# Performance work log

Hardware: AMD Instinct MI355X
Metric: run time of the kernel (lower is better)

Reference implementation:

```python
import jax, jax.numpy as jnp
import numpy as np

# NF4 quantization levels (16 entries) from NF4Quantizer
NF4_LEVELS = jnp.array([
    -1.0, -0.6961928009986877, -0.5250730514526367, -0.39491748809814453,
    -0.28444138169288635, -0.18477343022823334, -0.09105003625154495, 0.0,
    0.07958029955625534, 0.16093020141124725, 0.24611230194568634,
    0.33791524171829224, 0.44070982933044434, 0.5626170039176941,
    0.7229568362236023, 1.0], dtype=jnp.float32)

OUT_F, IN_F = 4096, 4096
B, S = 2, 512

def setup_inputs() -> dict:
    key = jax.random.key(0)
    k1, k2, k3, k4, k5 = jax.random.split(key, 5)
    x = jax.random.normal(k1, (B, S, IN_F), dtype=jnp.float32)
    w0 = jax.random.normal(k2, (OUT_F, IN_F), dtype=jnp.float32) * 0.02
    nf4_idx = jax.random.randint(k3, (OUT_F, IN_F), 0, 16, dtype=jnp.int32)
    scale = jax.random.uniform(k4, (1,), dtype=jnp.float32) * 0.1 + 0.01
    zero_point = jax.random.normal(k5, (1,), dtype=jnp.float32) * 0.01
    return {"x": x, "w0": w0, "nf4_idx": nf4_idx, "scale": scale,
            "zero_point": zero_point}

def reference(x, w0, nf4_idx, scale, zero_point):
    # NF4 dequantize: look up level values, then affine (quantized*scale + zp)
    q = NF4_LEVELS[nf4_idx]                      # [out, in] float32
    deq_w = q * scale + zero_point               # dequantized adaptor weight
    # frozen base linear + dequantized low-rank-adaptor linear (QLoRA-style)
    base = jnp.einsum('bsi,oi->bso', x, w0)
    adapt = jnp.einsum('bsi,oi->bso', x, deq_w)
    return base + adapt
```

## Files before the change

### kernel.cpp

```cpp
#include <hip/hip_runtime.h>
#include <hip/hip_bf16.h>
#include <stdint.h>

#define MDIM 1024
#define NDIM 4096
#define KDIM 4096

#define BM 128
#define BN 128
#define BK 64

typedef __attribute__((ext_vector_type(4))) float f32x4;
typedef __attribute__((ext_vector_type(4))) float float4v;
typedef __attribute__((ext_vector_type(4))) int int4v;
typedef __attribute__((ext_vector_type(4))) unsigned int uint4v;
typedef __attribute__((ext_vector_type(8))) short short8;

#define GLOBAL_AS __attribute__((address_space(1)))
#define LDS_AS __attribute__((address_space(3)))

#define HARD_BARRIER() do {                               \
    __builtin_amdgcn_sched_barrier(0);                    \
    asm volatile("s_waitcnt lgkmcnt(0)" ::: "memory");    \
    __builtin_amdgcn_s_barrier();                         \
    asm volatile("" ::: "memory");                        \
    __builtin_amdgcn_sched_barrier(0);                    \
} while (0)

__device__ __constant__ float c_nf4[16] = {
    -1.0f, -0.6961928009986877f, -0.5250730514526367f, -0.39491748809814453f,
    -0.28444138169288635f, -0.18477343022823334f, -0.09105003625154495f, 0.0f,
    0.07958029955625534f, 0.16093020141124725f, 0.24611230194568634f,
    0.33791524171829224f, 0.44070982933044434f, 0.5626170039176941f,
    0.7229568362236023f, 1.0f};

__device__ __forceinline__ unsigned bf16_rne(float f) {
    unsigned u = __float_as_uint(f);
    return (u + 0x7fffu + ((u >> 16) & 1u)) >> 16;
}

#define W_BLOCKS ((NDIM * KDIM) / (256 * 8))
#define X_BLOCKS ((MDIM * KDIM) / (256 * 8))

__global__ __launch_bounds__(256) void prep_kernel(
    const float* __restrict__ x, const float* __restrict__ w0,
    const int* __restrict__ nf4_idx, const float* __restrict__ scale_p,
    const float* __restrict__ zp_p, __hip_bfloat16* __restrict__ Wc,
    __hip_bfloat16* __restrict__ xb)
{
    const int lane = threadIdx.x & 63;
    if (blockIdx.x < W_BLOCKS) {
        const float scale = scale_p[0];
        const float zp = zp_p[0];
        const int tab = __float_as_int(c_nf4[lane & 15] * scale + zp);
        const size_t base = ((size_t)blockIdx.x * 256 + threadIdx.x) * 8;
        int4v i0 = *(const int4v*)(nf4_idx + base);
        int4v i1 = *(const int4v*)(nf4_idx + base + 4);
        float4v w_0 = *(const float4v*)(w0 + base);
        float4v w_1 = *(const float4v*)(w0 + base + 4);
        unsigned r[8];
#pragma unroll
        for (int j = 0; j < 4; j++) {
            float q = __int_as_float(__builtin_amdgcn_ds_bpermute(i0[j] * 4, tab));
            r[j] = bf16_rne(w_0[j] + q);
        }
#pragma unroll
        for (int j = 0; j < 4; j++) {
            float q = __int_as_float(__builtin_amdgcn_ds_bpermute(i1[j] * 4, tab));
            r[4 + j] = bf16_rne(w_1[j] + q);
        }
        uint4v st;
        st.x = r[0] | (r[1] << 16);
        st.y = r[2] | (r[3] << 16);
        st.z = r[4] | (r[5] << 16);
        st.w = r[6] | (r[7] << 16);
        *(uint4v*)((unsigned short*)Wc + base) = st;
    } else {
        const size_t base = ((size_t)(blockIdx.x - W_BLOCKS) * 256 + threadIdx.x) * 8;
        float4v a0 = *(const float4v*)(x + base);
        float4v a1 = *(const float4v*)(x + base + 4);
        uint4v st;
        st.x = bf16_rne(a0[0]) | (bf16_rne(a0[1]) << 16);
        st.y = bf16_rne(a0[2]) | (bf16_rne(a0[3]) << 16);
        st.z = bf16_rne(a1[0]) | (bf16_rne(a1[1]) << 16);
        st.w = bf16_rne(a1[2]) | (bf16_rne(a1[3]) << 16);
        *(uint4v*)((unsigned short*)xb + base) = st;
    }
}

__global__ __launch_bounds__(512) void gemm_kernel(
    const __hip_bfloat16* __restrict__ A,
    const __hip_bfloat16* __restrict__ B,
    float* __restrict__ C)
{
    __shared__ __hip_bfloat16 sm[4][2][BM * BK];

    const int tid = threadIdx.x;
    const int lane = tid & 63;
    const int w = tid >> 6;
    const int wr = w >> 2;
    const int wc = (w >> 1) & 1;
    const int wk = w & 1;

    const int bid = blockIdx.x;
    const int orig = (bid & 7) * 32 + (bid >> 3);
    const int mtile = orig & 7;
    const int ntile = orig >> 3;

    const int s_subrow = lane >> 3;
    const int s_chunkpos = lane & 7;
    int s_row[2], s_goff[2];
#pragma unroll
    for (int j = 0; j < 2; j++) {
        int row = w * 16 + j * 8 + s_subrow;
        s_row[j] = row;
        s_goff[j] = (s_chunkpos ^ (row & 7)) * 8;
    }

#define STAGE(buf, kt) do {                                                        \
    _Pragma("unroll")                                                              \
    for (int j = 0; j < 2; j++) {                                                  \
        const __hip_bfloat16* ga = A + (size_t)(mtile * BM + s_row[j]) * KDIM      \
                                     + (kt) * BK + s_goff[j];                      \
        __builtin_amdgcn_global_load_lds((const GLOBAL_AS void*)ga,                \
            (LDS_AS void*)&sm[buf][0][(w * 16 + j * 8) * BK], 16, 0, 0);           \
        const __hip_bfloat16* gb = B + (size_t)(ntile * BN + s_row[j]) * KDIM      \
                                     + (kt) * BK + s_goff[j];                      \
        __builtin_amdgcn_global_load_lds((const GLOBAL_AS void*)gb,                \
            (LDS_AS void*)&sm[buf][1][(w * 16 + j * 8) * BK], 16, 0, 0);           \
    }                                                                              \
} while (0)

    int a_off[4], b_off[4];
#pragma unroll
    for (int m = 0; m < 4; m++) {
        int row = wr * 64 + m * 16 + (lane & 15);
        int c = wk * 4 + (lane >> 4);
        a_off[m] = row * BK + (c ^ (row & 7)) * 8;
    }
#pragma unroll
    for (int n = 0; n < 4; n++) {
        int row = wc * 64 + n * 16 + (lane & 15);
        int c = wk * 4 + (lane >> 4);
        b_off[n] = row * BK + (c ^ (row & 7)) * 8;
    }

    f32x4 acc[4][4] = {};

#define COMPUTE(buf) do {                                                          \
    short8 af[4], bfv[4];                                                          \
    _Pragma("unroll")                                                              \
    for (int m = 0; m < 4; m++)                                                    \
        af[m] = *(const short8*)&sm[buf][0][a_off[m]];                             \
    _Pragma("unroll")                                                              \
    for (int n = 0; n < 4; n++)                                                    \
        bfv[n] = *(const short8*)&sm[buf][1][b_off[n]];                            \
    _Pragma("unroll")                                                              \
    for (int m = 0; m < 4; m++)                                                    \
        _Pragma("unroll")                                                          \
        for (int n = 0; n < 4; n++)                                                \
            acc[m][n] = __builtin_amdgcn_mfma_f32_16x16x32_bf16(                   \
                af[m], bfv[n], acc[m][n], 0, 0, 0);                                \
} while (0)

    const int NT = KDIM / BK;
    STAGE(0, 0);
    STAGE(1, 1);

    for (int t = 0; t < NT; t++) {
        const int cur = t & 3;
        if (t + 2 < NT) {
            STAGE((t + 2) & 3, t + 2);
            asm volatile("s_waitcnt vmcnt(8)" ::: "memory");
        } else if (t + 1 < NT) {
            asm volatile("s_waitcnt vmcnt(4)" ::: "memory");
        } else {
            asm volatile("s_waitcnt vmcnt(0)" ::: "memory");
        }
        HARD_BARRIER();
        COMPUTE(cur);
    }

    HARD_BARRIER();
    float* red = (float*)&sm[0][0][0];
    const int pair = wr * 2 + wc;
    if (wk == 1) {
#pragma unroll
        for (int m = 0; m < 4; m++) {
#pragma unroll
            for (int n = 0; n < 4; n++) {
                *(f32x4*)&red[pair * 4096 + (m * 4 + n) * 256 + lane * 4] =
                    acc[m][n];
            }
        }
    }
    HARD_BARRIER();
    if (wk == 0) {
        const int rbase = mtile * BM + wr * 64 + ((lane >> 4) << 2);
        const int cbase = ntile * BN + wc * 64 + (lane & 15);
#pragma unroll
        for (int m = 0; m < 4; m++) {
#pragma unroll
            for (int n = 0; n < 4; n++) {
                f32x4 other =
                    *(const f32x4*)&red[pair * 4096 + (m * 4 + n) * 256 + lane * 4];
                f32x4 v = acc[m][n] + other;
#pragma unroll
                for (int r = 0; r < 4; r++) {
                    C[(size_t)(rbase + m * 16 + r) * NDIM + cbase + n * 16] = v[r];
                }
            }
        }
    }
#undef STAGE
#undef COMPUTE
}

__global__ void fallback_kernel(const float* __restrict__ x,
                                const float* __restrict__ w0,
                                const int* __restrict__ nf4_idx,
                                const float* __restrict__ sp,
                                const float* __restrict__ zpp,
                                float* __restrict__ out)
{
    __shared__ float As[16][16], Bs[16][17];
    const int tx = threadIdx.x, ty = threadIdx.y;
    const int n0 = blockIdx.x * 16, m0 = blockIdx.y * 16;
    const float s = sp[0], zp = zpp[0];
    float acc = 0.0f;
    for (int k0 = 0; k0 < KDIM; k0 += 16) {
        As[ty][tx] = x[(size_t)(m0 + ty) * KDIM + k0 + tx];
        int id = nf4_idx[(size_t)(n0 + ty) * KDIM + k0 + tx];
        Bs[ty][tx] = w0[(size_t)(n0 + ty) * KDIM + k0 + tx] + c_nf4[id] * s + zp;
        __syncthreads();
#pragma unroll
        for (int j = 0; j < 16; j++) acc += As[ty][j] * Bs[tx][j];
        __syncthreads();
    }
    out[(size_t)(m0 + ty) * NDIM + n0 + tx] = acc;
}

extern "C" void kernel_launch(void* const* d_in, const int* in_sizes, int n_in,
                              void* d_out, int out_size, void* d_ws, size_t ws_size,
                              hipStream_t stream) {
    const float* x = (const float*)d_in[0];
    const float* w0 = (const float*)d_in[1];
    const int* nf4_idx = (const int*)d_in[2];
    const float* scale = (const float*)d_in[3];
    const float* zp = (const float*)d_in[4];
    float* out = (float*)d_out;

    const size_t wc_bytes = (size_t)NDIM * KDIM * 2;
    const size_t xb_bytes = (size_t)MDIM * KDIM * 2;

    if (ws_size >= wc_bytes + xb_bytes) {
        __hip_bfloat16* Wc = (__hip_bfloat16*)d_ws;
        __hip_bfloat16* xb = (__hip_bfloat16*)((char*)d_ws + wc_bytes);
        prep_kernel<<<W_BLOCKS + X_BLOCKS, 256, 0, stream>>>(
            x, w0, nf4_idx, scale, zp, Wc, xb);
        gemm_kernel<<<(MDIM / BM) * (NDIM / BN), 512, 0, stream>>>(xb, Wc, out);
    } else {
        fallback_kernel<<<dim3(NDIM / 16, MDIM / 16), dim3(16, 16), 0, stream>>>(
            x, w0, nf4_idx, scale, zp, out);
    }
}
```

Measured before the change: 66.55 us.

## Pre-swizzle operands into MFMA fragment layout and load fragments directly from global

The prep kernel now writes bf16 W and x in a tiled layout that matches the MFMA fragment order (16-row by 8-element units). The GEMM kernel drops its LDS staging, swizzle and per-step barriers and instead loads short8 fragments directly from global into registers with a 4-deep software prefetch. LDS is used only for the final split-K reduction, and launch bounds now request 2 blocks per CU. The risks are higher register pressure from 32 fragment registers plus accumulators, and no LDS reuse, so every wave reads its fragments from global/L2.

```diff
diff --git a/kernel.cpp b/kernel.cpp
--- a/kernel.cpp
+++ b/kernel.cpp
@@ -8,7 +8,6 @@
 
 #define BM 128
 #define BN 128
-#define BK 64
 
 typedef __attribute__((ext_vector_type(4))) float f32x4;
 typedef __attribute__((ext_vector_type(4))) float float4v;
@@ -54,6 +53,11 @@
         const float zp = zp_p[0];
         const int tab = __float_as_int(c_nf4[lane & 15] * scale + zp);
         const size_t base = ((size_t)blockIdx.x * 256 + threadIdx.x) * 8;
+        const int row = (int)(base >> 12);
+        const int k8 = (int)((base >> 3) & 511);
+        const int kc = k8 >> 2, hi = k8 & 3;
+        const size_t unit =
+            ((size_t)(row >> 4) * 128 + kc) * 64 + hi * 16 + (row & 15);
         int4v i0 = *(const int4v*)(nf4_idx + base);
         int4v i1 = *(const int4v*)(nf4_idx + base + 4);
         float4v w_0 = *(const float4v*)(w0 + base);
@@ -74,9 +78,14 @@
         st.y = r[2] | (r[3] << 16);
         st.z = r[4] | (r[5] << 16);
         st.w = r[6] | (r[7] << 16);
-        *(uint4v*)((unsigned short*)Wc + base) = st;
+        *(uint4v*)((unsigned short*)Wc + unit * 8) = st;
     } else {
         const size_t base = ((size_t)(blockIdx.x - W_BLOCKS) * 256 + threadIdx.x) * 8;
+        const int row = (int)(base >> 12);
+        const int k8 = (int)((base >> 3) & 511);
+        const int kc = k8 >> 2, hi = k8 & 3;
+        const size_t unit =
+            ((size_t)(row >> 4) * 128 + kc) * 64 + hi * 16 + (row & 15);
         float4v a0 = *(const float4v*)(x + base);
         float4v a1 = *(const float4v*)(x + base + 4);
         uint4v st;
@@ -84,16 +93,16 @@
         st.y = bf16_rne(a0[2]) | (bf16_rne(a0[3]) << 16);
         st.z = bf16_rne(a1[0]) | (bf16_rne(a1[1]) << 16);
         st.w = bf16_rne(a1[2]) | (bf16_rne(a1[3]) << 16);
-        *(uint4v*)((unsigned short*)xb + base) = st;
-    }
-}
-
-__global__ __launch_bounds__(512) void gemm_kernel(
+        *(uint4v*)((unsigned short*)xb + unit * 8) = st;
+    }
+}
+
+__global__ __launch_bounds__(512, 2) void gemm_kernel(
     const __hip_bfloat16* __restrict__ A,
     const __hip_bfloat16* __restrict__ B,
     float* __restrict__ C)
 {
-    __shared__ __hip_bfloat16 sm[4][2][BM * BK];
+    __shared__ float red[4 * 4096];
 
     const int tid = threadIdx.x;
     const int lane = tid & 63;
@@ -107,82 +116,50 @@
     const int mtile = orig & 7;
     const int ntile = orig >> 3;
 
-    const int s_subrow = lane >> 3;
-    const int s_chunkpos = lane & 7;
-    int s_row[2], s_goff[2];
-#pragma unroll
-    for (int j = 0; j < 2; j++) {
-        int row = w * 16 + j * 8 + s_subrow;
-        s_row[j] = row;
-        s_goff[j] = (s_chunkpos ^ (row & 7)) * 8;
-    }
-
-#define STAGE(buf, kt) do {                                                        \
-    _Pragma("unroll")                                                              \
-    for (int j = 0; j < 2; j++) {                                                  \
-        const __hip_bfloat16* ga = A + (size_t)(mtile * BM + s_row[j]) * KDIM      \
-                                     + (kt) * BK + s_goff[j];                      \
-        __builtin_amdgcn_global_load_lds((const GLOBAL_AS void*)ga,                \
-            (LDS_AS void*)&sm[buf][0][(w * 16 + j * 8) * BK], 16, 0, 0);           \
-        const __hip_bfloat16* gb = B + (size_t)(ntile * BN + s_row[j]) * KDIM      \
-                                     + (kt) * BK + s_goff[j];                      \
-        __builtin_amdgcn_global_load_lds((const GLOBAL_AS void*)gb,                \
-            (LDS_AS void*)&sm[buf][1][(w * 16 + j * 8) * BK], 16, 0, 0);           \
-    }                                                                              \
+    const short8* Af = (const short8*)A;
+    const short8* Bf = (const short8*)B;
+
+    int au[4], bu[4];
+#pragma unroll
+    for (int m = 0; m < 4; m++)
+        au[m] = ((mtile * 8 + wr * 4 + m) * 128 + wk * 64) * 64 + lane;
+#pragma unroll
+    for (int n = 0; n < 4; n++)
+        bu[n] = ((ntile * 8 + wc * 4 + n) * 128 + wk * 64) * 64 + lane;
+
+    f32x4 acc[4][4] = {};
+    short8 fa0[4], fb0[4], fa1[4], fb1[4], fa2[4], fb2[4], fa3[4], fb3[4];
+
+#define LOADF(fa, fb, t) do {                                                 \
+    _Pragma("unroll")                                                         \
+    for (int m = 0; m < 4; m++) fa[m] = Af[au[m] + (t) * 64];                 \
+    _Pragma("unroll")                                                         \
+    for (int n = 0; n < 4; n++) fb[n] = Bf[bu[n] + (t) * 64];                 \
 } while (0)
 
-    int a_off[4], b_off[4];
-#pragma unroll
-    for (int m = 0; m < 4; m++) {
-        int row = wr * 64 + m * 16 + (lane & 15);
-        int c = wk * 4 + (lane >> 4);
-        a_off[m] = row * BK + (c ^ (row & 7)) * 8;
-    }
-#pragma unroll
-    for (int n = 0; n < 4; n++) {
-        int row = wc * 64 + n * 16 + (lane & 15);
-        int c = wk * 4 + (lane >> 4);
-        b_off[n] = row * BK + (c ^ (row & 7)) * 8;
-    }
-
-    f32x4 acc[4][4] = {};
-
-#define COMPUTE(buf) do {                                                          \
-    short8 af[4], bfv[4];                                                          \
-    _Pragma("unroll")                                                              \
-    for (int m = 0; m < 4; m++)                                                    \
-        af[m] = *(const short8*)&sm[buf][0][a_off[m]];                             \
-    _Pragma("unroll")                                                              \
-    for (int n = 0; n < 4; n++)                                                    \
-        bfv[n] = *(const short8*)&sm[buf][1][b_off[n]];                            \
-    _Pragma("unroll")                                                              \
-    for (int m = 0; m < 4; m++)                                                    \
-        _Pragma("unroll")                                                          \
-        for (int n = 0; n < 4; n++)                                                \
-            acc[m][n] = __builtin_amdgcn_mfma_f32_16x16x32_bf16(                   \
-                af[m], bfv[n], acc[m][n], 0, 0, 0);                                \
+#define MF(fa, fb) do {                                                       \
+    _Pragma("unroll")                                                         \
+    for (int m = 0; m < 4; m++)                                               \
+        _Pragma("unroll")                                                     \
+        for (int n = 0; n < 4; n++)                                           \
+            acc[m][n] = __builtin_amdgcn_mfma_f32_16x16x32_bf16(              \
+                fa[m], fb[n], acc[m][n], 0, 0, 0);                            \
 } while (0)
 
-    const int NT = KDIM / BK;
-    STAGE(0, 0);
-    STAGE(1, 1);
-
-    for (int t = 0; t < NT; t++) {
-        const int cur = t & 3;
-        if (t + 2 < NT) {
-            STAGE((t + 2) & 3, t + 2);
-            asm volatile("s_waitcnt vmcnt(8)" ::: "memory");
-        } else if (t + 1 < NT) {
-            asm volatile("s_waitcnt vmcnt(4)" ::: "memory");
-        } else {
-            asm volatile("s_waitcnt vmcnt(0)" ::: "memory");
-        }
-        HARD_BARRIER();
-        COMPUTE(cur);
-    }
-
-    HARD_BARRIER();
-    float* red = (float*)&sm[0][0][0];
+    LOADF(fa0, fb0, 0);
+    LOADF(fa1, fb1, 1);
+    LOADF(fa2, fb2, 2);
+    for (int t = 0; t < 64; t += 4) {
+        LOADF(fa3, fb3, t + 3);
+        MF(fa0, fb0);
+        if (t + 4 < 64) LOADF(fa0, fb0, t + 4);
+        MF(fa1, fb1);
+        if (t + 5 < 64) LOADF(fa1, fb1, t + 5);
+        MF(fa2, fb2);
+        if (t + 6 < 64) LOADF(fa2, fb2, t + 6);
+        MF(fa3, fb3);
+    }
+
     const int pair = wr * 2 + wc;
     if (wk == 1) {
 #pragma unroll
@@ -212,8 +189,8 @@
             }
         }
     }
-#undef STAGE
-#undef COMPUTE
+#undef LOADF
+#undef MF
 }
 
 __global__ void fallback_kernel(const float* __restrict__ x,
```

Result: slower. 94.86 us (+42.5%).
